# Kernel optimization log

Hardware: AMD Instinct MI355X
Metric: run time of the kernel (lower is better)

Reference implementation:

```python
import jax, jax.numpy as jnp
import numpy as np

B, D, H1, H2 = 512, 1024, 512, 128

def setup_inputs() -> dict:
    key = jax.random.key(0)
    ks = jax.random.split(key, 3)
    x = jax.random.normal(ks[0], (B, D), dtype=jnp.float32)
    W1 = jax.random.normal(ks[1], (H1, D), dtype=jnp.float32)
    W2 = jax.random.normal(ks[2], (H2, H1), dtype=jnp.float32)
    b1 = jnp.full((H1,), 0.1, dtype=jnp.float32)
    b2 = jnp.full((H2,), 0.1, dtype=jnp.float32)
    b3 = jnp.full((H1,), 0.1, dtype=jnp.float32)
    b_r = jnp.full((D,), 0.1, dtype=jnp.float32)
    return {"x": x, "W1": W1, "b1": b1, "W2": W2, "b2": b2, "b3": b3, "b_r": b_r}

def reference(x, W1, b1, W2, b2, b3, b_r):
    # encoder
    c1 = jax.nn.sigmoid(x @ W1.T + b1)          # [B, H1]
    c2 = jax.nn.sigmoid(c1 @ W2.T + b2)         # [B, H2]
    # decoder (tied weights)
    c3 = jax.nn.sigmoid(c2 @ W2 + b3)           # [B, H1]
    recover = c3 @ W1 + b_r                     # [B, D]
    # Jacobian of code w.r.t. x, batched (replaces per-sample diag+matmul loop):
    # Jac[b] = diag(c2'(b)) @ W2 @ diag(c1'(b)) @ W1
    s1p = c1 * (1.0 - c1)                       # [B, H1]
    s2p = c2 * (1.0 - c2)                       # [B, H2]
    M = s2p[:, :, None] * W2[None, :, :] * s1p[:, None, :]   # [B, H2, H1]
    Jac = jnp.einsum('bhk,kd->bhd', M, W1)      # [B, H2, D]
    return (recover, c2, Jac)
```

## Files before the change

### kernel.cpp

```cpp
#include <hip/hip_runtime.h>


typedef _Float16 f16x8 __attribute__((ext_vector_type(8)));
typedef _Float16 f16x4 __attribute__((ext_vector_type(4)));
typedef float    f32x4 __attribute__((ext_vector_type(4)));
typedef float    f32x2 __attribute__((ext_vector_type(2)));

__device__ __forceinline__ void gld_lds16(const _Float16* src, _Float16* dst_wave_uniform) {
    __builtin_amdgcn_global_load_lds((const __attribute__((address_space(1))) unsigned int*)src,
                                     (__attribute__((address_space(3))) unsigned int*)dst_wave_uniform,
                                     16, 0, 0);
}

__device__ __forceinline__ void prep_dev(int bx, const float* __restrict__ W1,
                                         const float* __restrict__ W2,
                                         _Float16* __restrict__ W1T,
                                         _Float16* __restrict__ W2h) {
    if (bx < 512) {
        __shared__ float tile[32][33];
        int dt = (bx & 31) * 32, kt = (bx >> 5) * 32;
        int tx = threadIdx.x & 31, ty = threadIdx.x >> 5;
        #pragma unroll
        for (int r = 0; r < 32; r += 8)
            tile[ty + r][tx] = W1[(kt + ty + r) * 1024 + dt + tx];
        __syncthreads();
        #pragma unroll
        for (int r = 0; r < 32; r += 8)
            W1T[(size_t)(dt + ty + r) * 512 + kt + tx] = (_Float16)tile[tx][ty + r];
    } else {
        int i = (bx - 512) * 1024 + threadIdx.x * 4;
        f32x4 v = *(const f32x4*)(W2 + i);
        f16x4 h;
        h.x = (_Float16)v.x; h.y = (_Float16)v.y; h.z = (_Float16)v.z; h.w = (_Float16)v.w;
        *(f16x4*)(W2h + i) = h;
    }
}

template <int EPI, bool TRANSB>
__device__ void gemm_dev(const float* __restrict__ A, const float* __restrict__ Bm,
                         const float* __restrict__ bias,
                         float* __restrict__ C, float* __restrict__ Cd,
                         _Float16* __restrict__ Ch,
                         int M, int N, int K, int m0, int n0) {
    __shared__ __align__(16) float As[32][34];
    __shared__ __align__(16) float Bs[32][68];
    const int tid = threadIdx.x, tx = tid & 15, ty = tid >> 4;
    const int ka  = tid & 31, ma  = tid >> 5;
    const int kbt = tid & 31, nbt = tid >> 5;
    const int nbf = tid & 63, kbf = tid >> 6;
    float acc[2][4] = {};
    float rA[4], rB[8];

    #pragma unroll
    for (int r = 0; r < 4; ++r) rA[r] = A[(size_t)(m0 + ma + 8 * r) * K + ka];
    if (TRANSB) {
        #pragma unroll
        for (int r = 0; r < 8; ++r) rB[r] = Bm[(size_t)(n0 + nbt + 8 * r) * K + kbt];
    } else {
        #pragma unroll
        for (int r = 0; r < 8; ++r) rB[r] = Bm[(size_t)(kbf + 4 * r) * N + n0 + nbf];
    }

    for (int k0 = 0; k0 < K; k0 += 32) {
        #pragma unroll
        for (int r = 0; r < 4; ++r) As[ka][ma + 8 * r] = rA[r];
        if (TRANSB) {
            #pragma unroll
            for (int r = 0; r < 8; ++r) Bs[kbt][nbt + 8 * r] = rB[r];
        } else {
            #pragma unroll
            for (int r = 0; r < 8; ++r) Bs[kbf + 4 * r][nbf] = rB[r];
        }
        const int k1 = k0 + 32;
        if (k1 < K) {
            #pragma unroll
            for (int r = 0; r < 4; ++r) rA[r] = A[(size_t)(m0 + ma + 8 * r) * K + k1 + ka];
            if (TRANSB) {
                #pragma unroll
                for (int r = 0; r < 8; ++r) rB[r] = Bm[(size_t)(n0 + nbt + 8 * r) * K + k1 + kbt];
            } else {
                #pragma unroll
                for (int r = 0; r < 8; ++r) rB[r] = Bm[(size_t)(k1 + kbf + 4 * r) * N + n0 + nbf];
            }
        }
        __syncthreads();
        #pragma unroll
        for (int k = 0; k < 32; ++k) {
            f32x2 av = *(const f32x2*)&As[k][ty * 2];
            f32x4 bv = *(const f32x4*)&Bs[k][tx * 4];
            #pragma unroll
            for (int i = 0; i < 2; ++i)
                #pragma unroll
                for (int j = 0; j < 4; ++j)
                    acc[i][j] += av[i] * bv[j];
        }
        __syncthreads();
    }

    #pragma unroll
    for (int i = 0; i < 2; ++i) {
        int row = m0 + ty * 2 + i;
        #pragma unroll
        for (int j = 0; j < 4; ++j) {
            int col = n0 + tx * 4 + j;
            float z = acc[i][j] + bias[col];
            float s = 1.f / (1.f + __expf(-z));
            if constexpr (EPI == 1) {
                C[(size_t)row * N + col]  = s;
                Cd[(size_t)row * N + col] = s * (1.f - s);
            } else {
                Ch[(size_t)row * N + col] = (_Float16)s;
            }
        }
    }
}

__device__ __forceinline__ void buildA_dev(int b, const float* __restrict__ W2,
                                           const float* __restrict__ s1p,
                                           const float* __restrict__ s2p,
                                           _Float16* __restrict__ A_all) {
    const int tid = threadIdx.x;
    __shared__ float S1[512];
    __shared__ float S2[128];
    S1[tid]       = s1p[(size_t)b * 512 + tid];
    S1[tid + 256] = s1p[(size_t)b * 512 + tid + 256];
    if (tid < 128) S2[tid] = s2p[(size_t)b * 128 + tid];
    __syncthreads();
    _Float16* out = A_all + (size_t)b * 65536;
    #pragma unroll 4
    for (int i = 0; i < 32; ++i) {
        int c = tid + 256 * i;
        int h = c >> 6, k8 = (c & 63) * 8;
        f32x4 w0 = *(const f32x4*)(W2 + h * 512 + k8);
        f32x4 w1 = *(const f32x4*)(W2 + h * 512 + k8 + 4);
        float s2 = S2[h];
        f16x8 o;
        o[0] = (_Float16)(s2 * w0.x * S1[k8 + 0]);
        o[1] = (_Float16)(s2 * w0.y * S1[k8 + 1]);
        o[2] = (_Float16)(s2 * w0.z * S1[k8 + 2]);
        o[3] = (_Float16)(s2 * w0.w * S1[k8 + 3]);
        o[4] = (_Float16)(s2 * w1.x * S1[k8 + 4]);
        o[5] = (_Float16)(s2 * w1.y * S1[k8 + 5]);
        o[6] = (_Float16)(s2 * w1.z * S1[k8 + 6]);
        o[7] = (_Float16)(s2 * w1.w * S1[k8 + 7]);
        *(f16x8*)(out + h * 512 + k8) = o;
    }
}

__global__ __launch_bounds__(256) void fused_prep_gemm1(const float* __restrict__ x,
                                                        const float* __restrict__ W1,
                                                        const float* __restrict__ b1,
                                                        const float* __restrict__ W2,
                                                        _Float16* __restrict__ W1T,
                                                        _Float16* __restrict__ W2h,
                                                        float* __restrict__ c1,
                                                        float* __restrict__ s1p) {
    int bx = blockIdx.x;
    if (bx < 128) {
        gemm_dev<1, true>(x, W1, b1, c1, s1p, nullptr, 512, 512, 1024,
                          (bx >> 3) * 32, (bx & 7) * 64);
    } else {
        prep_dev(bx - 128, W1, W2, W1T, W2h);
    }
}

__global__ __launch_bounds__(256) void gemm2_kernel(const float* __restrict__ c1,
                                                    const float* __restrict__ W2,
                                                    const float* __restrict__ b2,
                                                    float* __restrict__ out_c2,
                                                    float* __restrict__ s2p) {
    gemm_dev<1, true>(c1, W2, b2, out_c2, s2p, nullptr, 512, 128, 512,
                      blockIdx.y * 32, blockIdx.x * 64);
}

__global__ __launch_bounds__(256) void gemm3_kernel(const float* __restrict__ out_c2,
                                                    const float* __restrict__ W2,
                                                    const float* __restrict__ b3,
                                                    _Float16* __restrict__ c3h) {
    gemm_dev<2, false>(out_c2, W2, b3, nullptr, nullptr, c3h, 512, 512, 128,
                       (blockIdx.x >> 3) * 32, (blockIdx.x & 7) * 64);
}

__global__ __launch_bounds__(256) void fused_mid(const float* __restrict__ out_c2,
                                                 const float* __restrict__ W2,
                                                 const float* __restrict__ b3,
                                                 _Float16* __restrict__ c3h,
                                                 const float* __restrict__ s1p,
                                                 const float* __restrict__ s2p,
                                                 _Float16* __restrict__ A_all) {
    int bx = blockIdx.x;
    if (bx < 128) {
        gemm_dev<2, false>(out_c2, W2, b3, nullptr, nullptr, c3h, 512, 512, 128,
                           (bx >> 3) * 32, (bx & 7) * 64);
    } else {
        buildA_dev(bx - 128, W2, s1p, s2p, A_all);
    }
}

__global__ __launch_bounds__(256) void fused_mfma(const _Float16* __restrict__ c3h,
                                                  const _Float16* __restrict__ A_all,
                                                  const _Float16* __restrict__ W1T,
                                                  const float* __restrict__ br,
                                                  float* __restrict__ out_rec,
                                                  float* __restrict__ out_jac) {
    __shared__ __align__(16) _Float16 Asl[128 * 64];
    __shared__ __align__(16) _Float16 Bsl[128 * 64];
    __shared__ float Bias[128];

    const int bid = blockIdx.x;
    const _Float16* A;
    float* Out;
    int m0, n0;
    bool has_bias;
    if (bid < 32) {
        has_bias = true;
        A = c3h; Out = out_rec;
        n0 = (bid & 7) * 128; m0 = (bid >> 3) * 128;
    } else {
        int jid = bid - 32;
        int w = (jid & 7) * 512 + (jid >> 3);
        int z = w >> 3;
        has_bias = false;
        A = A_all + (size_t)z * 65536;
        Out = out_jac + (size_t)z * 131072;
        n0 = (w & 7) * 128; m0 = 0;
    }
    const int K = 512, Nn = 1024;
    const int tid = threadIdx.x;
    const int lane = tid & 63, wave = tid >> 6;
    const int wm = (wave >> 1) * 64, wn = (wave & 1) * 64;
    const int l15 = lane & 15, q = lane >> 4;

    if (tid < 128) Bias[tid] = has_bias ? br[n0 + tid] : 0.f;

    f32x4 acc[4][4];
    #pragma unroll
    for (int i = 0; i < 4; ++i)
        #pragma unroll
        for (int j = 0; j < 4; ++j) acc[i][j] = (f32x4){0.f, 0.f, 0.f, 0.f};

    const int rbase = wave * 8 + (lane >> 3);
    const int kof   = (lane & 7) * 8;

    for (int k0 = 0; k0 < K; k0 += 64) {
        #pragma unroll
        for (int r = 0; r < 4; ++r) {
            gld_lds16(A   + (size_t)(m0 + r * 32 + rbase) * K + k0 + kof, Asl + (r * 32 + wave * 8) * 64);
            gld_lds16(W1T + (size_t)(n0 + r * 32 + rbase) * K + k0 + kof, Bsl + (r * 32 + wave * 8) * 64);
        }
        __syncthreads();
        #pragma unroll
        for (int kk = 0; kk < 64; kk += 32) {
            f16x8 af[4], bf[4];
            #pragma unroll
            for (int i = 0; i < 4; ++i)
                af[i] = *(const f16x8*)(Asl + (wm + i * 16 + l15) * 64 + kk + q * 8);
            #pragma unroll
            for (int j = 0; j < 4; ++j)
                bf[j] = *(const f16x8*)(Bsl + (wn + j * 16 + l15) * 64 + kk + q * 8);
            #pragma unroll
            for (int i = 0; i < 4; ++i)
                #pragma unroll
                for (int j = 0; j < 4; ++j)
                    acc[i][j] = __builtin_amdgcn_mfma_f32_16x16x32_f16(af[i], bf[j], acc[i][j], 0, 0, 0);
        }
        __syncthreads();
    }

    #pragma unroll
    for (int i = 0; i < 4; ++i) {
        #pragma unroll
        for (int rg = 0; rg < 4; ++rg) {
            int m = m0 + wm + i * 16 + q * 4 + rg;
            #pragma unroll
            for (int j = 0; j < 4; ++j) {
                int dcol = wn + j * 16 + l15;
                Out[(size_t)m * Nn + n0 + dcol] = acc[i][j][rg] + Bias[dcol];
            }
        }
    }
}

template <bool HAS_BIAS>
__global__ __launch_bounds__(256) void mfma_bt(const _Float16* __restrict__ Abase,
                                               const _Float16* __restrict__ Bmat,
                                               const float* __restrict__ bias,
                                               float* __restrict__ OutBase,
                                               int K, int N,
                                               long aBatch, long oBatch) {
    __shared__ __align__(16) _Float16 Asl[128 * 64];
    __shared__ __align__(16) _Float16 Bsl[128 * 64];
    __shared__ float Bias[128];
    const _Float16* A = Abase + (size_t)blockIdx.z * aBatch;
    float* Out = OutBase + (size_t)blockIdx.z * oBatch;
    const int m0 = blockIdx.y * 128, n0 = blockIdx.x * 128;
    const int tid = threadIdx.x;
    const int lane = tid & 63, wave = tid >> 6;
    const int wm = (wave >> 1) * 64, wn = (wave & 1) * 64;
    const int l15 = lane & 15, q = lane >> 4;

    if (HAS_BIAS && tid < 128) Bias[tid] = bias[n0 + tid];

    f32x4 acc[4][4];
    #pragma unroll
    for (int i = 0; i < 4; ++i)
        #pragma unroll
        for (int j = 0; j < 4; ++j) acc[i][j] = (f32x4){0.f, 0.f, 0.f, 0.f};

    const int rbase = wave * 8 + (lane >> 3);
    const int kof   = (lane & 7) * 8;

    for (int k0 = 0; k0 < K; k0 += 64) {
        #pragma unroll
        for (int r = 0; r < 4; ++r) {
            gld_lds16(A    + (size_t)(m0 + r * 32 + rbase) * K + k0 + kof, Asl + (r * 32 + wave * 8) * 64);
            gld_lds16(Bmat + (size_t)(n0 + r * 32 + rbase) * K + k0 + kof, Bsl + (r * 32 + wave * 8) * 64);
        }
        __syncthreads();
        #pragma unroll
        for (int kk = 0; kk < 64; kk += 32) {
            f16x8 af[4], bf[4];
            #pragma unroll
            for (int i = 0; i < 4; ++i)
                af[i] = *(const f16x8*)(Asl + (wm + i * 16 + l15) * 64 + kk + q * 8);
            #pragma unroll
            for (int j = 0; j < 4; ++j)
                bf[j] = *(const f16x8*)(Bsl + (wn + j * 16 + l15) * 64 + kk + q * 8);
            #pragma unroll
            for (int i = 0; i < 4; ++i)
                #pragma unroll
                for (int j = 0; j < 4; ++j)
                    acc[i][j] = __builtin_amdgcn_mfma_f32_16x16x32_f16(af[i], bf[j], acc[i][j], 0, 0, 0);
        }
        __syncthreads();
    }

    #pragma unroll
    for (int i = 0; i < 4; ++i) {
        #pragma unroll
        for (int rg = 0; rg < 4; ++rg) {
            int m = m0 + wm + i * 16 + q * 4 + rg;
            #pragma unroll
            for (int j = 0; j < 4; ++j) {
                int dcol = wn + j * 16 + l15;
                float v = acc[i][j][rg];
                if (HAS_BIAS) v += Bias[dcol];
                Out[(size_t)m * N + n0 + dcol] = v;
            }
        }
    }
}

__global__ __launch_bounds__(256) void jac_kernel(const _Float16* __restrict__ W2h,
                                                  const _Float16* __restrict__ W1T,
                                                  const float* __restrict__ s1p,
                                                  const float* __restrict__ s2p,
                                                  float* __restrict__ Jac) {
    __shared__ __align__(16) _Float16 Asl[128 * 64];
    __shared__ __align__(16) _Float16 Bsl[128 * 64];
    __shared__ float Ssl[128];
    const int b  = blockIdx.y;
    const int n0 = blockIdx.x * 128;
    const int tid = threadIdx.x;
    const int lane = tid & 63, wave = tid >> 6;
    const int wm = (wave >> 1) * 64, wn = (wave & 1) * 64;
    const int l15 = lane & 15, q = lane >> 4;

    if (tid < 128) Ssl[tid] = s2p[b * 128 + tid];

    f32x4 acc[4][4];
    #pragma unroll
    for (int i = 0; i < 4; ++i)
        #pragma unroll
        for (int j = 0; j < 4; ++j) acc[i][j] = (f32x4){0.f, 0.f, 0.f, 0.f};

    const int ah  = tid >> 4;
    const int akq = (tid & 15) * 4;
    const int rbase = wave * 8 + (lane >> 3);
    const int kof   = (lane & 7) * 8;

    for (int k0 = 0; k0 < 512; k0 += 64) {
        f32x4 s4 = *(const f32x4*)(s1p + (size_t)b * 512 + k0 + akq);
        f16x4 s4h;
        s4h.x = (_Float16)s4.x; s4h.y = (_Float16)s4.y;
        s4h.z = (_Float16)s4.z; s4h.w = (_Float16)s4.w;
        #pragma unroll
        for (int r = 0; r < 8; ++r) {
            int h = ah + r * 16;
            f16x4 w4 = *(const f16x4*)(W2h + (size_t)h * 512 + k0 + akq);
            *(f16x4*)(Asl + h * 64 + akq) = w4 * s4h;
        }
        #pragma unroll
        for (int r = 0; r < 4; ++r)
            gld_lds16(W1T + (size_t)(n0 + r * 32 + rbase) * 512 + k0 + kof,
                      Bsl + (r * 32 + wave * 8) * 64);
        __syncthreads();

        #pragma unroll
        for (int kk = 0; kk < 64; kk += 32) {
            f16x8 af[4], bf[4];
            #pragma unroll
            for (int i = 0; i < 4; ++i)
                af[i] = *(const f16x8*)(Asl + (wm + i * 16 + l15) * 64 + kk + q * 8);
            #pragma unroll
            for (int j = 0; j < 4; ++j)
                bf[j] = *(const f16x8*)(Bsl + (wn + j * 16 + l15) * 64 + kk + q * 8);
            #pragma unroll
            for (int i = 0; i < 4; ++i)
                #pragma unroll
                for (int j = 0; j < 4; ++j)
                    acc[i][j] = __builtin_amdgcn_mfma_f32_16x16x32_f16(af[i], bf[j], acc[i][j], 0, 0, 0);
        }
        __syncthreads();
    }

    float* outb = Jac + (size_t)b * (128 * 1024);
    #pragma unroll
    for (int i = 0; i < 4; ++i) {
        #pragma unroll
        for (int rg = 0; rg < 4; ++rg) {
            int h = wm + i * 16 + q * 4 + rg;
            float s = Ssl[h];
            #pragma unroll
            for (int j = 0; j < 4; ++j) {
                int d = n0 + wn + j * 16 + l15;
                outb[(size_t)h * 1024 + d] = acc[i][j][rg] * s;
            }
        }
    }
}

extern "C" void kernel_launch(void* const* d_in, const int* in_sizes, int n_in,
                              void* d_out, int out_size, void* d_ws, size_t ws_size,
                              hipStream_t stream) {
    const float* x  = (const float*)d_in[0];
    const float* W1 = (const float*)d_in[1];
    const float* b1 = (const float*)d_in[2];
    const float* W2 = (const float*)d_in[3];
    const float* b2 = (const float*)d_in[4];
    const float* b3 = (const float*)d_in[5];
    const float* br = (const float*)d_in[6];

    float* out_rec = (float*)d_out;
    float* out_c2  = out_rec + 512 * 1024;
    float* out_jac = out_c2 + 512 * 128;

    char* ws = (char*)d_ws;
    _Float16* W1T   = (_Float16*)(ws);
    _Float16* W2h   = (_Float16*)(ws + 0x100000);
    float*    c1    = (float*)(ws + 0x120000);
    float*    s1p   = (float*)(ws + 0x220000);
    float*    s2p   = (float*)(ws + 0x320000);
    _Float16* c3h   = (_Float16*)(ws + 0x360000);
    _Float16* A_all = (_Float16*)(ws + 0x400000);
    const bool big_ws = ws_size >= (size_t)0x4400000;

    fused_prep_gemm1<<<704, 256, 0, stream>>>(x, W1, b1, W2, W1T, W2h, c1, s1p);
    gemm2_kernel<<<dim3(2, 16), 256, 0, stream>>>(c1, W2, b2, out_c2, s2p);
    if (big_ws) {
        fused_mid<<<640, 256, 0, stream>>>(out_c2, W2, b3, c3h, s1p, s2p, A_all);
        fused_mfma<<<4128, 256, 0, stream>>>(c3h, A_all, W1T, br, out_rec, out_jac);
    } else {
        gemm3_kernel<<<128, 256, 0, stream>>>(out_c2, W2, b3, c3h);
        mfma_bt<true><<<dim3(8, 4, 1), 256, 0, stream>>>(c3h, W1T, br, out_rec, 512, 1024, 0, 0);
        jac_kernel<<<dim3(8, 512), 256, 0, stream>>>(W2h, W1T, s1p, s2p, out_jac);
    }
}
```

Baseline: 436.1 us.

## Rewrite fused MFMA GEMM with 256x256 tiles, double-buffered LDS and swizzle

Replaces the 128x128-tile fused reconstruction/Jacobian GEMM with a 512-thread kernel that computes 256x256 output tiles. It double-buffers LDS with async global_load_lds prefetch two stages ahead, gated by explicit vmcnt waits and barriers. An XOR swizzle on the LDS column offset aims to cut bank conflicts, and s_setprio raises wave priority around the MFMA bursts. The larger tiles give more reuse per LDS byte, but the kernel uses about 128KB of LDS per block, which limits occupancy.

```diff
diff --git a/kernel.cpp b/kernel.cpp
--- a/kernel.cpp
+++ b/kernel.cpp
@@ -197,85 +197,125 @@
     }
 }
 
-__global__ __launch_bounds__(256) void fused_mfma(const _Float16* __restrict__ c3h,
-                                                  const _Float16* __restrict__ A_all,
-                                                  const _Float16* __restrict__ W1T,
-                                                  const float* __restrict__ br,
-                                                  float* __restrict__ out_rec,
-                                                  float* __restrict__ out_jac) {
-    __shared__ __align__(16) _Float16 Asl[128 * 64];
-    __shared__ __align__(16) _Float16 Bsl[128 * 64];
-    __shared__ float Bias[128];
+__global__ __launch_bounds__(512, 2) void jac8_kernel(const _Float16* __restrict__ c3h,
+                                                      const _Float16* __restrict__ A_all,
+                                                      const _Float16* __restrict__ W1T,
+                                                      const float* __restrict__ br,
+                                                      float* __restrict__ out_rec,
+                                                      float* __restrict__ out_jac) {
+    __shared__ __align__(16) _Float16 Asl[2][256 * 64];
+    __shared__ __align__(16) _Float16 Bsl[2][256 * 64];
+    __shared__ float BiasS[256];
 
     const int bid = blockIdx.x;
     const _Float16* A;
     float* Out;
     int m0, n0;
     bool has_bias;
-    if (bid < 32) {
+    if (bid < 8) {
         has_bias = true;
         A = c3h; Out = out_rec;
-        n0 = (bid & 7) * 128; m0 = (bid >> 3) * 128;
+        m0 = (bid >> 2) * 256; n0 = (bid & 3) * 256;
     } else {
-        int jid = bid - 32;
-        int w = (jid & 7) * 512 + (jid >> 3);
-        int z = w >> 3;
+        int jid = bid - 8;
+        int w = (jid & 7) * 128 + (jid >> 3);
         has_bias = false;
-        A = A_all + (size_t)z * 65536;
-        Out = out_jac + (size_t)z * 131072;
-        n0 = (w & 7) * 128; m0 = 0;
-    }
-    const int K = 512, Nn = 1024;
+        A = A_all; Out = out_jac;
+        m0 = (w >> 2) * 256; n0 = (w & 3) * 256;
+    }
+
     const int tid = threadIdx.x;
     const int lane = tid & 63, wave = tid >> 6;
-    const int wm = (wave >> 1) * 64, wn = (wave & 1) * 64;
+    const int wm = (wave >> 2) * 128, wn = (wave & 3) * 64;
     const int l15 = lane & 15, q = lane >> 4;
 
-    if (tid < 128) Bias[tid] = has_bias ? br[n0 + tid] : 0.f;
-
-    f32x4 acc[4][4];
-    #pragma unroll
-    for (int i = 0; i < 4; ++i)
+    if (tid < 256) BiasS[tid] = has_bias ? br[n0 + tid] : 0.f;
+
+    const int srow = wave * 8 + (lane >> 3);
+    const int skof = ((lane & 7) ^ (lane >> 3)) * 8;
+    const _Float16* Abase = A   + (size_t)m0 * 512;
+    const _Float16* Bbase = W1T + (size_t)n0 * 512;
+
+    auto STAGE = [&](int t) {
+        const int buf = t & 1;
+        const int kb = t * 64;
+        #pragma unroll
+        for (int r = 0; r < 4; ++r)
+            gld_lds16(Abase + (size_t)(r * 64 + srow) * 512 + kb + skof,
+                      &Asl[buf][(r * 64 + wave * 8) * 64]);
+        #pragma unroll
+        for (int r = 0; r < 4; ++r)
+            gld_lds16(Bbase + (size_t)(r * 64 + srow) * 512 + kb + skof,
+                      &Bsl[buf][(r * 64 + wave * 8) * 64]);
+    };
+
+    f32x4 acc[8][4];
+    #pragma unroll
+    for (int i = 0; i < 8; ++i)
         #pragma unroll
         for (int j = 0; j < 4; ++j) acc[i][j] = (f32x4){0.f, 0.f, 0.f, 0.f};
 
-    const int rbase = wave * 8 + (lane >> 3);
-    const int kof   = (lane & 7) * 8;
-
-    for (int k0 = 0; k0 < K; k0 += 64) {
-        #pragma unroll
-        for (int r = 0; r < 4; ++r) {
-            gld_lds16(A   + (size_t)(m0 + r * 32 + rbase) * K + k0 + kof, Asl + (r * 32 + wave * 8) * 64);
-            gld_lds16(W1T + (size_t)(n0 + r * 32 + rbase) * K + k0 + kof, Bsl + (r * 32 + wave * 8) * 64);
-        }
-        __syncthreads();
-        #pragma unroll
-        for (int kk = 0; kk < 64; kk += 32) {
-            f16x8 af[4], bf[4];
-            #pragma unroll
-            for (int i = 0; i < 4; ++i)
-                af[i] = *(const f16x8*)(Asl + (wm + i * 16 + l15) * 64 + kk + q * 8);
+    STAGE(0);
+    STAGE(1);
+
+    const int swz = (l15 & 7) * 8;
+
+    #pragma unroll 1
+    for (int t = 0; t < 8; ++t) {
+        if (t < 7) asm volatile("s_waitcnt vmcnt(8)" ::: "memory");
+        else       asm volatile("s_waitcnt vmcnt(0)" ::: "memory");
+        __builtin_amdgcn_s_barrier();
+        const int buf = t & 1;
+        const _Float16* As = &Asl[buf][0];
+        const _Float16* Bs = &Bsl[buf][0];
+
+        f16x8 a0[8], b0[4];
+        #pragma unroll
+        for (int i = 0; i < 8; ++i)
+            a0[i] = *(const f16x8*)(As + (wm + i * 16 + l15) * 64 + ((0 + q * 8) ^ swz));
+        #pragma unroll
+        for (int j = 0; j < 4; ++j)
+            b0[j] = *(const f16x8*)(Bs + (wn + j * 16 + l15) * 64 + ((0 + q * 8) ^ swz));
+
+        __builtin_amdgcn_s_setprio(1);
+        #pragma unroll
+        for (int i = 0; i < 8; ++i)
             #pragma unroll
             for (int j = 0; j < 4; ++j)
-                bf[j] = *(const f16x8*)(Bsl + (wn + j * 16 + l15) * 64 + kk + q * 8);
-            #pragma unroll
-            for (int i = 0; i < 4; ++i)
-                #pragma unroll
-                for (int j = 0; j < 4; ++j)
-                    acc[i][j] = __builtin_amdgcn_mfma_f32_16x16x32_f16(af[i], bf[j], acc[i][j], 0, 0, 0);
-        }
-        __syncthreads();
-    }
-
-    #pragma unroll
-    for (int i = 0; i < 4; ++i) {
+                acc[i][j] = __builtin_amdgcn_mfma_f32_16x16x32_f16(a0[i], b0[j], acc[i][j], 0, 0, 0);
+        __builtin_amdgcn_s_setprio(0);
+
+        f16x8 a1[8], b1[4];
+        #pragma unroll
+        for (int i = 0; i < 8; ++i)
+            a1[i] = *(const f16x8*)(As + (wm + i * 16 + l15) * 64 + ((32 + q * 8) ^ swz));
+        #pragma unroll
+        for (int j = 0; j < 4; ++j)
+            b1[j] = *(const f16x8*)(Bs + (wn + j * 16 + l15) * 64 + ((32 + q * 8) ^ swz));
+
+        asm volatile("s_waitcnt lgkmcnt(0)" ::: "memory");
+        __builtin_amdgcn_s_barrier();
+        if (t + 2 < 8) STAGE(t + 2);
+        __builtin_amdgcn_sched_barrier(0);
+
+        __builtin_amdgcn_s_setprio(1);
+        #pragma unroll
+        for (int i = 0; i < 8; ++i)
+            #pragma unroll
+            for (int j = 0; j < 4; ++j)
+                acc[i][j] = __builtin_amdgcn_mfma_f32_16x16x32_f16(a1[i], b1[j], acc[i][j], 0, 0, 0);
+        __builtin_amdgcn_s_setprio(0);
+    }
+
+    #pragma unroll
+    for (int i = 0; i < 8; ++i) {
         #pragma unroll
         for (int rg = 0; rg < 4; ++rg) {
             int m = m0 + wm + i * 16 + q * 4 + rg;
             #pragma unroll
             for (int j = 0; j < 4; ++j) {
-                int dcol = wn + j * 16 + l15;
-                Out[(size_t)m * Nn + n0 + dcol] = acc[i][j][rg] + Bias[dcol];
+                int col = wn + j * 16 + l15;
+                Out[(size_t)m * 1024 + n0 + col] = acc[i][j][rg] + BiasS[col];
             }
         }
     }
@@ -459,7 +499,7 @@
     gemm2_kernel<<<dim3(2, 16), 256, 0, stream>>>(c1, W2, b2, out_c2, s2p);
     if (big_ws) {
         fused_mid<<<640, 256, 0, stream>>>(out_c2, W2, b3, c3h, s1p, s2p, A_all);
-        fused_mfma<<<4128, 256, 0, stream>>>(c3h, A_all, W1T, br, out_rec, out_jac);
+        jac8_kernel<<<1032, 512, 0, stream>>>(c3h, A_all, W1T, br, out_rec, out_jac);
     } else {
         gemm3_kernel<<<128, 256, 0, stream>>>(out_c2, W2, b3, c3h);
         mfma_bt<true><<<dim3(8, 4, 1), 256, 0, stream>>>(c3h, W1T, br, out_rec, 512, 1024, 0, 0);
```

After: 431.6 us. About the same (-1.0%).
